# Kernel tuning notes

Hardware: AMD Instinct MI355X
Metric: run time of the kernel (lower is better)

Reference implementation:

```python
import jax, jax.numpy as jnp
import numpy as np

N_NODES = 20000
N_EDGES = 320000
N_GRAPHS = 32
C = 256
L = 4
IN_DIM = 739
EDGE_DIM = 2 * C + 6
LN_EPS = 1e-5


def _layernorm(x, g, b):
    mu = jnp.mean(x, axis=-1, keepdims=True)
    var = jnp.mean(jnp.square(x - mu), axis=-1, keepdims=True)
    return (x - mu) * jax.lax.rsqrt(var + LN_EPS) * g + b


def setup_inputs() -> dict:
    key = jax.random.key(0)
    ks = jax.random.split(key, 20)
    d = {}
    d["x"] = jax.random.normal(ks[0], (N_NODES, IN_DIM), jnp.float32)
    d["x_pos"] = jax.random.normal(ks[1], (N_NODES, 3), jnp.float32)
    d["edge_index"] = jax.random.randint(ks[2], (2, N_EDGES), 0, N_NODES, jnp.int32)
    d["batch"] = jnp.sort(jax.random.randint(ks[3], (N_NODES,), 0, N_GRAPHS, jnp.int32))
    s = 0.02
    d["dense_w"] = jax.random.normal(ks[4], (IN_DIM, C), jnp.float32) * s
    d["dense_b"] = jnp.zeros((C,), jnp.float32)
    d["d1_w"] = jax.random.normal(ks[5], (L, C, C), jnp.float32) * s
    d["d1_b"] = jnp.zeros((L, C), jnp.float32)
    d["ln1_g"] = jnp.ones((L, EDGE_DIM), jnp.float32)
    d["ln1_b"] = jnp.zeros((L, EDGE_DIM), jnp.float32)
    d["w1_w"] = jax.random.normal(ks[6], (L, EDGE_DIM, 4), jnp.float32) * s
    d["w1_b"] = jnp.zeros((L, 4), jnp.float32)
    d["ln2_g"] = jnp.ones((L, 4), jnp.float32)
    d["ln2_b"] = jnp.zeros((L, 4), jnp.float32)
    d["w2_w"] = jax.random.normal(ks[7], (L, 4, 1), jnp.float32) * s
    d["w2_b"] = jnp.zeros((L, 1), jnp.float32)
    d["d2_w"] = jax.random.normal(ks[8], (L, C, C), jnp.float32) * s
    d["d2_b"] = jnp.zeros((L, C), jnp.float32)
    d["head_w"] = jax.random.normal(ks[9], (C, 1), jnp.float32) * s
    d["head_b"] = jnp.zeros((1,), jnp.float32)
    return d


def reference(x, x_pos, edge_index, batch, dense_w, dense_b, d1_w, d1_b,
              ln1_g, ln1_b, w1_w, w1_b, ln2_g, ln2_b, w2_w, w2_b,
              d2_w, d2_b, head_w, head_b):
    n = x.shape[0]
    src, dst = edge_index[0], edge_index[1]
    h = x @ dense_w + dense_b  # [N, C]
    for l in range(d1_w.shape[0]):
        # message: dense1 -> GELU (dropout is identity in eval)
        m = jax.nn.gelu(h @ d1_w[l] + d1_b[l], approximate=False)  # [N, C]
        sx = m[src]                                                # [E, C]
        # edge-MLP input: [src_x, dst_x, src_pos, dst_pos]
        e = jnp.concatenate([sx, m[dst], x_pos[src], x_pos[dst]], axis=-1)  # [E, 2C+6]
        e = _layernorm(e, ln1_g[l], ln1_b[l])
        e = jax.nn.gelu(e @ w1_w[l] + w1_b[l], approximate=False)  # [E, 4]
        e = _layernorm(e, ln2_g[l], ln2_b[l])
        w = jax.nn.sigmoid(e @ w2_w[l] + w2_b[l])                  # [E, 1]
        agg = jax.ops.segment_sum(sx * w, dst, num_segments=n)     # [N, C]
        # update: dense2 -> GELU
        h = jax.nn.gelu(agg @ d2_w[l] + d2_b[l], approximate=False)
    # global mean pool over graphs
    sums = jax.ops.segment_sum(h, batch, num_segments=N_GRAPHS)           # [G, C]
    cnts = jax.ops.segment_sum(jnp.ones((n, 1), h.dtype), batch, num_segments=N_GRAPHS)
    pooled = sums / jnp.maximum(cnts, 1.0)
    return pooled @ head_w + head_b  # [G, 1]
```

## Files before the change

kernel.cpp:

```cpp
#include <hip/hip_runtime.h>
#include <math.h>

#define N_NODES 20000
#define N_EDGES 320000
#define N_GRAPHS 32
#define CDIM 256
#define IN_DIMV 739
#define KPAD_DENSE 768
#define ED_DIM 518
#define NLAYERS 4
#define LN_EPS 1e-5f
#define SCAN_BLOCKS ((N_NODES + 255) / 256)

typedef _Float16 f16x8 __attribute__((ext_vector_type(8)));
typedef _Float16 f16x4 __attribute__((ext_vector_type(4)));
typedef float f32x4 __attribute__((ext_vector_type(4)));

__device__ __forceinline__ float gelu_exact(float x) {
    return 0.5f * x * (1.f + erff(x * 0.7071067811865475f));
}

__device__ __forceinline__ void gll16(const void* g, void* l) {
    __builtin_amdgcn_global_load_lds((const __attribute__((address_space(1))) void*)g,
                                     (__attribute__((address_space(3))) void*)l, 16, 0, 0);
}

__global__ __launch_bounds__(256)
void prep_all(const float* __restrict__ ln1_g, const float* __restrict__ ln1_b,
              const float* __restrict__ w1_w, float* __restrict__ cw,
              float* __restrict__ SgSb,
              const float* __restrict__ dense_w, _Float16* __restrict__ wt_dense,
              const float* __restrict__ d1_w, const float* __restrict__ d2_w,
              _Float16* __restrict__ wt_sq, int* __restrict__ deg,
              float* __restrict__ sdot) {
    __shared__ float smem[2048 + 64];
    int b = blockIdx.x, tid = threadIdx.x;
    if (b < 79) {
        int i = b * 256 + tid;
        if (i < N_NODES) deg[i] = 0;
    } else if (b < 83) {
        int l = b - 79;
        float sg[4] = {0, 0, 0, 0}, sb[4] = {0, 0, 0, 0};
        for (int i = tid; i < ED_DIM; i += 256) {
            float g = ln1_g[l * ED_DIM + i];
            float bb = ln1_b[l * ED_DIM + i];
            float4 w = *(const float4*)&w1_w[(size_t)(l * ED_DIM + i) * 4];
            float4 c = make_float4(g * w.x, g * w.y, g * w.z, g * w.w);
            *(float4*)&cw[(size_t)(l * ED_DIM + i) * 4] = c;
            sg[0] += c.x; sg[1] += c.y; sg[2] += c.z; sg[3] += c.w;
            sb[0] += bb * w.x; sb[1] += bb * w.y; sb[2] += bb * w.z; sb[3] += bb * w.w;
        }
        for (int c = 0; c < 4; c++) { smem[tid * 8 + c] = sg[c]; smem[tid * 8 + 4 + c] = sb[c]; }
        __syncthreads();
        for (int s = 128; s > 0; s >>= 1) {
            if (tid < s)
                for (int c = 0; c < 8; c++) smem[tid * 8 + c] += smem[(tid + s) * 8 + c];
            __syncthreads();
        }
        if (tid < 8) SgSb[l * 8 + tid] = smem[tid];
    } else if (b < 275) {
        int q = b - 83;
        int kt = q >> 3, nt = q & 7;
        int i = tid >> 5, j = tid & 31;
        float* T = smem;
#pragma unroll
        for (int ii = 0; ii < 4; ii++) {
            int k = kt * 32 + i + ii * 8;
            T[(i + ii * 8) * 33 + j] = (k < IN_DIMV) ? dense_w[(size_t)k * 256 + nt * 32 + j] : 0.f;
        }
        __syncthreads();
#pragma unroll
        for (int ii = 0; ii < 4; ii++) {
            int n = nt * 32 + i + ii * 8;
            wt_dense[(size_t)n * KPAD_DENSE + kt * 32 + j] = (_Float16)T[j * 33 + i + ii * 8];
        }
    } else if (b < 787) {
        int q = b - 275;
        int z = q >> 6, kt = (q >> 3) & 7, nt = q & 7;
        const float* W = (z < 4) ? d1_w + (size_t)z * 65536 : d2_w + (size_t)(z - 4) * 65536;
        _Float16* O = wt_sq + (size_t)z * 65536;
        int i = tid >> 5, j = tid & 31;
        float* T = smem;
#pragma unroll
        for (int ii = 0; ii < 4; ii++)
            T[(i + ii * 8) * 33 + j] = W[(size_t)(kt * 32 + i + ii * 8) * 256 + nt * 32 + j];
        __syncthreads();
#pragma unroll
        for (int ii = 0; ii < 4; ii++)
            O[(size_t)(nt * 32 + i + ii * 8) * 256 + kt * 32 + j] = (_Float16)T[j * 33 + i + ii * 8];
    } else {
        int i = (b - 787) * 256 + tid;
        if (i < N_NODES) sdot[i] = 0.f;
    }
}

__global__ void hist_gstart_kernel(const int* __restrict__ ei, const int* __restrict__ batch,
                                   int* __restrict__ deg, int* __restrict__ gstart) {
    int e = blockIdx.x * 256 + threadIdx.x;
    if (e < N_EDGES) atomicAdd(&deg[ei[N_EDGES + e]], 1);
    if (e < N_NODES) {
        int b = batch[e];
        int bprev = (e == 0) ? -1 : batch[e - 1];
        for (int g = bprev + 1; g <= b; g++) gstart[g] = e;
        if (e == N_NODES - 1)
            for (int g = b + 1; g <= N_GRAPHS; g++) gstart[g] = N_NODES;
    }
}

__global__ __launch_bounds__(256)
void scan1_kernel(const int* __restrict__ deg, int* __restrict__ bsum) {
    __shared__ int red[256];
    int t = threadIdx.x;
    int i = blockIdx.x * 256 + t;
    red[t] = (i < N_NODES) ? deg[i] : 0;
    __syncthreads();
    for (int s = 128; s > 0; s >>= 1) {
        if (t < s) red[t] += red[t + s];
        __syncthreads();
    }
    if (t == 0) bsum[blockIdx.x] = red[0];
}

__global__ __launch_bounds__(128)
void scan2_kernel(const int* __restrict__ bsum, int* __restrict__ boff) {
    __shared__ int s[128];
    int t = threadIdx.x;
    int v = (t < SCAN_BLOCKS) ? bsum[t] : 0;
    s[t] = v;
    __syncthreads();
    for (int off = 1; off < 128; off <<= 1) {
        int o = (t >= off) ? s[t - off] : 0;
        __syncthreads();
        s[t] += o;
        __syncthreads();
    }
    if (t < SCAN_BLOCKS) boff[t] = s[t] - v;
}

__global__ __launch_bounds__(256)
void scan3_kernel(const int* __restrict__ deg, const int* __restrict__ boff,
                  int* __restrict__ row_start, int* __restrict__ cursor) {
    __shared__ int s[256];
    int t = threadIdx.x;
    int i = blockIdx.x * 256 + t;
    int v = (i < N_NODES) ? deg[i] : 0;
    s[t] = v;
    __syncthreads();
    for (int off = 1; off < 256; off <<= 1) {
        int o = (t >= off) ? s[t - off] : 0;
        __syncthreads();
        s[t] += o;
        __syncthreads();
    }
    int base = boff[blockIdx.x];
    int excl = base + s[t] - v;
    if (i < N_NODES) {
        row_start[i] = excl;
        cursor[i] = excl;
    }
    if (i == N_NODES - 1) row_start[N_NODES] = base + s[t];
}

__global__ void scatter_kernel(const int* __restrict__ ei, int* __restrict__ cursor,
                               int* __restrict__ csr_src, int* __restrict__ slot) {
    int e = blockIdx.x * 256 + threadIdx.x;
    if (e < N_EDGES) {
        int d = ei[N_EDGES + e];
        int pos = atomicAdd(&cursor[d], 1);
        csr_src[pos] = ei[e];
        slot[e] = pos;
    }
}

template <int KSTEPS, int AK, bool AFP32, bool GELU_ACT, bool DOT>
__global__ __launch_bounds__(256)
void gemm_v2(const void* __restrict__ Av, const _Float16* __restrict__ Bt,
             const float* __restrict__ bias, _Float16* __restrict__ C,
             const float* __restrict__ head_w, float* __restrict__ sdot) {
    constexpr int BSTR = KSTEPS * 64;
    __shared__ __align__(16) _Float16 Bs[3 * 128 * 64];
    __shared__ __align__(16) _Float16 As[(AFP32 ? 2 : 3) * 64 * 64];

    const int tid = threadIdx.x;
    const int row0 = blockIdx.x * 64;
    const int col0 = blockIdx.y * 128;
    const int wave = tid >> 6, lane = tid & 63;
    const int quad = lane >> 4, lrow = lane & 15;
    const int wrow = wave >> 1, wcol = wave & 1;

    const int sr = tid >> 3;
    const int scb = (tid & 7) << 4;
    const int srcCb = scb ^ ((sr & 7) << 4);

    const char* bsrc[4];
#pragma unroll
    for (int i = 0; i < 4; ++i)
        bsrc[i] = (const char*)Bt + (size_t)(col0 + i * 32 + sr) * (BSTR * 2) + srcCb;
    char* const bdst = (char*)&Bs[0] + tid * 16;

    const char* asrc[2];
    const float* afsrc[2];
    char* const adst = (char*)&As[0] + tid * 16;
    char* const adstw = (char*)&As[0] + sr * 128 + srcCb;
#pragma unroll
    for (int i = 0; i < 2; ++i) {
        int ar = row0 + i * 32 + sr;
        ar = (ar < N_NODES) ? ar : (N_NODES - 1);
        asrc[i] = (const char*)Av + (size_t)ar * (AK * 2) + srcCb;
        afsrc[i] = (const float*)Av + (size_t)ar * AK + (scb >> 1);
    }

    const int swz = ((lrow & 7) << 4) ^ (quad << 4);
    const int aro0 = (wrow * 32 + lrow) * 128;
    const int aro1 = aro0 + 2048;
    int bro[4];
#pragma unroll
    for (int t = 0; t < 4; ++t) bro[t] = (wcol * 64 + t * 16 + lrow) * 128;

    f32x4 acc[2][4];
#pragma unroll
    for (int i = 0; i < 2; ++i)
#pragma unroll
        for (int t = 0; t < 4; ++t) acc[i][t] = (f32x4){0.f, 0.f, 0.f, 0.f};

    float av[2][2][8];

    auto stage = [&](int j) {
        const int kb = j * 128;
        const int b3 = (j % 3) * 16384;
#pragma unroll
        for (int i = 0; i < 4; ++i) gll16(bsrc[i] + kb, bdst + b3 + i * 4096);
        if constexpr (!AFP32) {
            const int a3 = (j % 3) * 8192;
#pragma unroll
            for (int i = 0; i < 2; ++i) gll16(asrc[i] + kb, adst + a3 + i * 4096);
        } else {
            const int k0 = j * 64;
            const int p = j & 1;
            if ((j + 1) * 64 <= AK) {
#pragma unroll
                for (int jj = 0; jj < 8; ++jj) {
                    av[p][0][jj] = afsrc[0][k0 + jj];
                    av[p][1][jj] = afsrc[1][k0 + jj];
                }
            } else {
                const int kbase = k0 + (scb >> 1);
#pragma unroll
                for (int jj = 0; jj < 8; ++jj) {
                    av[p][0][jj] = (kbase + jj < AK) ? afsrc[0][k0 + jj] : 0.f;
                    av[p][1][jj] = (kbase + jj < AK) ? afsrc[1][k0 + jj] : 0.f;
                }
            }
        }
    };

    auto awrite = [&](int j) {
        if constexpr (AFP32) {
            const int ab = (j & 1) * 8192;
            const int p = j & 1;
            f16x8 v0, v1;
#pragma unroll
            for (int jj = 0; jj < 8; ++jj) {
                v0[jj] = (_Float16)av[p][0][jj];
                v1[jj] = (_Float16)av[p][1][jj];
            }
            *(f16x8*)(adstw + ab) = v0;
            *(f16x8*)(adstw + ab + 4096) = v1;
        }
    };

    auto compute = [&](int k) {
        const char* pa = (const char*)&As[0] + (AFP32 ? (k & 1) : (k % 3)) * 8192;
        const char* pb = (const char*)&Bs[0] + (k % 3) * 16384;
        __builtin_amdgcn_s_setprio(1);
#pragma unroll
        for (int h = 0; h < 2; ++h) {
            const int cbs = (h << 6) ^ swz;
            f16x8 af0 = *(const f16x8*)(pa + aro0 + cbs);
            f16x8 af1 = *(const f16x8*)(pa + aro1 + cbs);
#pragma unroll
            for (int t = 0; t < 4; ++t) {
                f16x8 bf = *(const f16x8*)(pb + bro[t] + cbs);
                acc[0][t] = __builtin_amdgcn_mfma_f32_16x16x32_f16(af0, bf, acc[0][t], 0, 0, 0);
                acc[1][t] = __builtin_amdgcn_mfma_f32_16x16x32_f16(af1, bf, acc[1][t], 0, 0, 0);
            }
        }
        __builtin_amdgcn_s_setprio(0);
    };

    stage(0);
    if constexpr (AFP32) {
        asm volatile("s_waitcnt vmcnt(0)" ::: "memory");
        __builtin_amdgcn_sched_barrier(0);
        awrite(0);
        stage(1);
        asm volatile("s_waitcnt lgkmcnt(0)" ::: "memory");
    } else {
        stage(1);
        asm volatile("s_waitcnt vmcnt(6) lgkmcnt(0)" ::: "memory");
    }
    __builtin_amdgcn_sched_barrier(0);
    __builtin_amdgcn_s_barrier();
    __builtin_amdgcn_sched_barrier(0);

#pragma unroll
    for (int k = 0; k < KSTEPS; ++k) {
        if (k + 2 < KSTEPS) stage(k + 2);
        compute(k);
        if (k + 1 < KSTEPS) {
            if (k + 2 < KSTEPS) {
                if constexpr (AFP32)
                    asm volatile("s_waitcnt vmcnt(8) lgkmcnt(0)" ::: "memory");
                else
                    asm volatile("s_waitcnt vmcnt(6) lgkmcnt(0)" ::: "memory");
            } else {
                asm volatile("s_waitcnt vmcnt(0) lgkmcnt(0)" ::: "memory");
            }
            __builtin_amdgcn_sched_barrier(0);
            if constexpr (AFP32) {
                awrite(k + 1);
                asm volatile("s_waitcnt lgkmcnt(0)" ::: "memory");
                __builtin_amdgcn_sched_barrier(0);
            }
            __builtin_amdgcn_s_barrier();
            __builtin_amdgcn_sched_barrier(0);
        }
    }

    const int orow = row0 + wrow * 32 + quad * 4;
    const int ocolb = col0 + wcol * 64 + lrow;
    if constexpr (DOT) {
        float dp0[4] = {0.f, 0.f, 0.f, 0.f}, dp1[4] = {0.f, 0.f, 0.f, 0.f};
#pragma unroll
        for (int t = 0; t < 4; ++t) {
            const int col = ocolb + t * 16;
            const float hw = head_w[col];
            const float bv = bias[col];
#pragma unroll
            for (int r = 0; r < 4; ++r) {
                dp0[r] += gelu_exact(acc[0][t][r] + bv) * hw;
                dp1[r] += gelu_exact(acc[1][t][r] + bv) * hw;
            }
        }
#pragma unroll
        for (int r = 0; r < 4; ++r) {
#pragma unroll
            for (int off = 1; off < 16; off <<= 1) {
                dp0[r] += __shfl_xor(dp0[r], off, 64);
                dp1[r] += __shfl_xor(dp1[r], off, 64);
            }
        }
        if (lrow == 0) {
#pragma unroll
            for (int r = 0; r < 4; ++r) {
                if (orow + r < N_NODES) atomicAdd(&sdot[orow + r], dp0[r]);
                if (orow + 16 + r < N_NODES) atomicAdd(&sdot[orow + 16 + r], dp1[r]);
            }
        }
    } else {
#pragma unroll
        for (int t = 0; t < 4; ++t) {
            const int col = ocolb + t * 16;
            const float bv = bias[col];
#pragma unroll
            for (int r = 0; r < 4; ++r) {
                float v0 = acc[0][t][r] + bv;
                float v1 = acc[1][t][r] + bv;
                if constexpr (GELU_ACT) { v0 = gelu_exact(v0); v1 = gelu_exact(v1); }
                if (orow + r < N_NODES)
                    C[(size_t)(orow + r) * 256 + col] = (_Float16)v0;
                if (orow + 16 + r < N_NODES)
                    C[(size_t)(orow + 16 + r) * 256 + col] = (_Float16)v1;
            }
        }
    }
}

__global__ __launch_bounds__(256)
void node_summary_kernel(const _Float16* __restrict__ m, const float* __restrict__ cw,
                         float* __restrict__ ns) {
    __shared__ __align__(16) float4 s_cw[512];
    int tid = threadIdx.x;
    for (int i = tid; i < 512; i += 256) s_cw[i] = *(const float4*)&cw[(size_t)i * 4];
    __syncthreads();
    int n = blockIdx.x * 4 + (tid >> 6);
    if (n >= N_NODES) return;
    int lane = tid & 63;
    f16x4 a4 = *(const f16x4*)&m[(size_t)n * CDIM + lane * 4];
    float av[4] = {(float)a4[0], (float)a4[1], (float)a4[2], (float)a4[3]};
    float Q1 = 0.f, Q2 = 0.f, P1[4] = {0, 0, 0, 0}, P2[4] = {0, 0, 0, 0};
#pragma unroll
    for (int j = 0; j < 4; j++) {
        Q1 += av[j];
        Q2 += av[j] * av[j];
        float4 c0 = s_cw[lane * 4 + j];
        float4 c1 = s_cw[256 + lane * 4 + j];
        P1[0] += av[j] * c0.x; P1[1] += av[j] * c0.y; P1[2] += av[j] * c0.z; P1[3] += av[j] * c0.w;
        P2[0] += av[j] * c1.x; P2[1] += av[j] * c1.y; P2[2] += av[j] * c1.z; P2[3] += av[j] * c1.w;
    }
#pragma unroll
    for (int off = 1; off < 64; off <<= 1) {
        Q1 += __shfl_xor(Q1, off, 64);
        Q2 += __shfl_xor(Q2, off, 64);
        P1[0] += __shfl_xor(P1[0], off, 64);
        P1[1] += __shfl_xor(P1[1], off, 64);
        P1[2] += __shfl_xor(P1[2], off, 64);
        P1[3] += __shfl_xor(P1[3], off, 64);
        P2[0] += __shfl_xor(P2[0], off, 64);
        P2[1] += __shfl_xor(P2[1], off, 64);
        P2[2] += __shfl_xor(P2[2], off, 64);
        P2[3] += __shfl_xor(P2[3], off, 64);
    }
    if (lane == 0) {
        float* p = &ns[(size_t)n * 12];
        *(float4*)p = make_float4(P1[0], P1[1], P1[2], P1[3]);
        *(float4*)(p + 4) = make_float4(P2[0], P2[1], P2[2], P2[3]);
        p[8] = Q1;
        p[9] = Q2;
    }
}

__global__ __launch_bounds__(256)
void edge_weight_kernel(const float* __restrict__ ns, const float* __restrict__ x_pos,
                        const int* __restrict__ ei, const float* __restrict__ cw,
                        const float* __restrict__ SgSb, const float* __restrict__ w1_b,
                        const float* __restrict__ ln2_g, const float* __restrict__ ln2_b,
                        const float* __restrict__ w2_w, const float* __restrict__ w2_b,
                        const int* __restrict__ slot, float* __restrict__ w_csr) {
    int e = blockIdx.x * 256 + threadIdx.x;
    if (e >= N_EDGES) return;
    int s = ei[e], d = ei[N_EDGES + e];
    const float* nss = &ns[(size_t)s * 12];
    const float* nsd = &ns[(size_t)d * 12];
    float4 p1 = *(const float4*)nss;
    float4 p2 = *(const float4*)(nsd + 4);
    float S1 = nss[8] + nsd[8];
    float S2 = nss[9] + nsd[9];
    float D[4] = {p1.x + p2.x, p1.y + p2.y, p1.z + p2.z, p1.w + p2.w};
    float ps[6];
    ps[0] = x_pos[(size_t)s * 3 + 0];
    ps[1] = x_pos[(size_t)s * 3 + 1];
    ps[2] = x_pos[(size_t)s * 3 + 2];
    ps[3] = x_pos[(size_t)d * 3 + 0];
    ps[4] = x_pos[(size_t)d * 3 + 1];
    ps[5] = x_pos[(size_t)d * 3 + 2];
#pragma unroll
    for (int k = 0; k < 6; k++) {
        S1 += ps[k];
        S2 += ps[k] * ps[k];
        float4 c = *(const float4*)&cw[(size_t)(512 + k) * 4];
        D[0] += ps[k] * c.x; D[1] += ps[k] * c.y; D[2] += ps[k] * c.z; D[3] += ps[k] * c.w;
    }
    const float inv = 1.f / 518.f;
    float mu = S1 * inv;
    float var = fmaf(-mu, mu, S2 * inv);
    float rstd = rsqrtf(var + LN_EPS);
    float t[4];
#pragma unroll
    for (int c = 0; c < 4; c++)
        t[c] = gelu_exact(rstd * (D[c] - mu * SgSb[c]) + SgSb[4 + c] + w1_b[c]);
    float mu2 = 0.25f * (t[0] + t[1] + t[2] + t[3]);
    float var2 = 0.25f * ((t[0] - mu2) * (t[0] - mu2) + (t[1] - mu2) * (t[1] - mu2) +
                          (t[2] - mu2) * (t[2] - mu2) + (t[3] - mu2) * (t[3] - mu2));
    float r2 = rsqrtf(var2 + LN_EPS);
    float z = w2_b[0];
#pragma unroll
    for (int c = 0; c < 4; c++)
        z += ((t[c] - mu2) * r2 * ln2_g[c] + ln2_b[c]) * w2_w[c];
    w_csr[slot[e]] = 1.f / (1.f + expf(-z));
}

__global__ __launch_bounds__(256)
void agg_kernel(const _Float16* __restrict__ m, const int* __restrict__ csr_src,
                const float* __restrict__ w_csr, const int* __restrict__ row_start,
                _Float16* __restrict__ agg) {
    int n = blockIdx.x * 4 + (threadIdx.x >> 6);
    if (n >= N_NODES) return;
    int lane = threadIdx.x & 63;
    int beg = row_start[n], end = row_start[n + 1];
    float a0 = 0.f, a1 = 0.f, a2 = 0.f, a3 = 0.f;
    int j = beg;
    for (; j + 8 <= end; j += 8) {
        int si[8];
        float wi[8];
#pragma unroll
        for (int u = 0; u < 8; u++) { si[u] = csr_src[j + u]; wi[u] = w_csr[j + u]; }
        f16x4 v[8];
#pragma unroll
        for (int u = 0; u < 8; u++) v[u] = *(const f16x4*)&m[(size_t)si[u] * CDIM + lane * 4];
#pragma unroll
        for (int u = 0; u < 8; u++) {
            a0 = fmaf(wi[u], (float)v[u][0], a0);
            a1 = fmaf(wi[u], (float)v[u][1], a1);
            a2 = fmaf(wi[u], (float)v[u][2], a2);
            a3 = fmaf(wi[u], (float)v[u][3], a3);
        }
    }
    for (; j < end; j++) {
        int s = csr_src[j];
        float w = w_csr[j];
        f16x4 v = *(const f16x4*)&m[(size_t)s * CDIM + lane * 4];
        a0 = fmaf(w, (float)v[0], a0);
        a1 = fmaf(w, (float)v[1], a1);
        a2 = fmaf(w, (float)v[2], a2);
        a3 = fmaf(w, (float)v[3], a3);
    }
    f16x4 o;
    o[0] = (_Float16)a0; o[1] = (_Float16)a1; o[2] = (_Float16)a2; o[3] = (_Float16)a3;
    *(f16x4*)&agg[(size_t)n * CDIM + lane * 4] = o;
}

__global__ __launch_bounds__(256)
void final_head_kernel(const float* __restrict__ sdot, const int* __restrict__ gstart,
                       const float* __restrict__ head_b, float* __restrict__ out) {
    int g = blockIdx.x;
    int t = threadIdx.x;
    int beg = gstart[g], end = gstart[g + 1];
    float s = 0.f;
    for (int i = beg + t; i < end; i += 256) s += sdot[i];
    __shared__ float red[256];
    red[t] = s;
    __syncthreads();
    for (int k = 128; k > 0; k >>= 1) {
        if (t < k) red[t] += red[t + k];
        __syncthreads();
    }
    if (t == 0) out[g] = red[0] / fmaxf((float)(end - beg), 1.f) + head_b[0];
}

extern "C" void kernel_launch(void* const* d_in, const int* in_sizes, int n_in,
                              void* d_out, int out_size, void* d_ws, size_t ws_size,
                              hipStream_t stream) {
    const float* x       = (const float*)d_in[0];
    const float* x_pos   = (const float*)d_in[1];
    const int*   ei      = (const int*)d_in[2];
    const int*   batch   = (const int*)d_in[3];
    const float* dense_w = (const float*)d_in[4];
    const float* dense_b = (const float*)d_in[5];
    const float* d1_w    = (const float*)d_in[6];
    const float* d1_b    = (const float*)d_in[7];
    const float* ln1_g   = (const float*)d_in[8];
    const float* ln1_b   = (const float*)d_in[9];
    const float* w1_w    = (const float*)d_in[10];
    const float* w1_b    = (const float*)d_in[11];
    const float* ln2_g   = (const float*)d_in[12];
    const float* ln2_b   = (const float*)d_in[13];
    const float* w2_w    = (const float*)d_in[14];
    const float* w2_b    = (const float*)d_in[15];
    const float* d2_w    = (const float*)d_in[16];
    const float* d2_b    = (const float*)d_in[17];
    const float* head_w  = (const float*)d_in[18];
    const float* head_b  = (const float*)d_in[19];
    float* out = (float*)d_out;

    _Float16* hbuf0 = (_Float16*)d_ws;
    _Float16* hbuf1 = hbuf0 + (size_t)N_NODES * CDIM;
    _Float16* wt_dense = hbuf1 + (size_t)N_NODES * CDIM;
    _Float16* wt_sq    = wt_dense + (size_t)256 * KPAD_DENSE;
    float* cw    = (float*)(wt_sq + (size_t)8 * 256 * 256);
    float* SgSb  = cw + (size_t)NLAYERS * ED_DIM * 4;
    float* ns    = SgSb + NLAYERS * 8;
    float* sdot  = ns + (size_t)N_NODES * 12;
    float* w_csr = sdot + N_NODES;
    int* gstart    = (int*)(w_csr + N_EDGES);
    int* deg       = gstart + N_GRAPHS + 1;
    int* row_start = deg + N_NODES;
    int* cursor    = row_start + N_NODES + 1;
    int* csr_src   = cursor + N_NODES;
    int* slot      = csr_src + N_EDGES;
    int* bsum      = slot + N_EDGES;
    int* boff      = bsum + SCAN_BLOCKS;

    prep_all<<<866, 256, 0, stream>>>(ln1_g, ln1_b, w1_w, cw, SgSb,
                                      dense_w, wt_dense, d1_w, d2_w, wt_sq, deg, sdot);

    hist_gstart_kernel<<<(N_EDGES + 255) / 256, 256, 0, stream>>>(ei, batch, deg, gstart);
    scan1_kernel<<<SCAN_BLOCKS, 256, 0, stream>>>(deg, bsum);
    scan2_kernel<<<1, 128, 0, stream>>>(bsum, boff);
    scan3_kernel<<<SCAN_BLOCKS, 256, 0, stream>>>(deg, boff, row_start, cursor);
    scatter_kernel<<<(N_EDGES + 255) / 256, 256, 0, stream>>>(ei, cursor, csr_src, slot);

    const dim3 G2((N_NODES + 63) / 64, 2);
    gemm_v2<12, IN_DIMV, true, false, false><<<G2, 256, 0, stream>>>(
        x, wt_dense, dense_b, hbuf0, nullptr, nullptr);

    _Float16* h = hbuf0;
    _Float16* other = hbuf1;
    for (int l = 0; l < NLAYERS; l++) {
        gemm_v2<4, CDIM, false, true, false><<<G2, 256, 0, stream>>>(
            h, wt_sq + (size_t)l * 65536, d1_b + l * CDIM, other, nullptr, nullptr);
        node_summary_kernel<<<(N_NODES + 3) / 4, 256, 0, stream>>>(
            other, cw + (size_t)l * ED_DIM * 4, ns);
        edge_weight_kernel<<<(N_EDGES + 255) / 256, 256, 0, stream>>>(
            ns, x_pos, ei, cw + (size_t)l * ED_DIM * 4, SgSb + l * 8, w1_b + l * 4,
            ln2_g + l * 4, ln2_b + l * 4, w2_w + l * 4, w2_b + l, slot, w_csr);
        agg_kernel<<<(N_NODES + 3) / 4, 256, 0, stream>>>(other, csr_src, w_csr, row_start, h);
        if (l < NLAYERS - 1) {
            gemm_v2<4, CDIM, false, true, false><<<G2, 256, 0, stream>>>(
                h, wt_sq + (size_t)(4 + l) * 65536, d2_b + l * CDIM, other, nullptr, nullptr);
        } else {
            gemm_v2<4, CDIM, false, true, true><<<G2, 256, 0, stream>>>(
                h, wt_sq + (size_t)(4 + l) * 65536, d2_b + l * CDIM, other, head_w, sdot);
        }
        _Float16* tmp = h; h = other; other = tmp;
    }

    final_head_kernel<<<N_GRAPHS, 256, 0, stream>>>(sdot, gstart, head_b, out);
}
```

Measured before the change: 554.5 us.

## Pre-convert x to padded fp16 and use direct-to-LDS loads in dense GEMM

Adds a separate kernel that converts the fp32 input features into a zero-padded fp16 buffer, so the first dense GEMM can stage A tiles with global_load_lds like the square GEMMs instead of doing register loads and in-kernel conversion. The GEMM template now takes a configurable pipeline depth, and the per-layer 256-wide GEMMs drop to double buffering. The conversion kernel adds an extra full read of x plus a write and re-read of the fp16 copy, and it uses per-element integer division.

```diff
diff --git a/kernel.cpp b/kernel.cpp
--- a/kernel.cpp
+++ b/kernel.cpp
@@ -23,6 +23,30 @@
 __device__ __forceinline__ void gll16(const void* g, void* l) {
     __builtin_amdgcn_global_load_lds((const __attribute__((address_space(1))) void*)g,
                                      (__attribute__((address_space(3))) void*)l, 16, 0, 0);
+}
+
+__global__ __launch_bounds__(256)
+void convert_x_kernel(const float* __restrict__ x, _Float16* __restrict__ xh) {
+    const int nquads = (N_NODES * IN_DIMV) / 4;
+    const int stride = gridDim.x * 256;
+    for (int q = blockIdx.x * 256 + threadIdx.x; q < nquads; q += stride) {
+        float4 v = ((const float4*)x)[q];
+        int base = q * 4;
+        float vv[4] = {v.x, v.y, v.z, v.w};
+#pragma unroll
+        for (int e = 0; e < 4; ++e) {
+            int idx = base + e;
+            int row = idx / IN_DIMV;
+            int col = idx - row * IN_DIMV;
+            xh[row * KPAD_DENSE + col] = (_Float16)vv[e];
+        }
+    }
+    const int npad = N_NODES * (KPAD_DENSE - IN_DIMV);
+    for (int p = blockIdx.x * 256 + threadIdx.x; p < npad; p += stride) {
+        int row = p / (KPAD_DENSE - IN_DIMV);
+        int col = IN_DIMV + (p - row * (KPAD_DENSE - IN_DIMV));
+        xh[row * KPAD_DENSE + col] = (_Float16)0.f;
+    }
 }
 
 __global__ __launch_bounds__(256)
@@ -172,14 +196,14 @@
     }
 }
 
-template <int KSTEPS, int AK, bool AFP32, bool GELU_ACT, bool DOT>
-__global__ __launch_bounds__(256)
-void gemm_v2(const void* __restrict__ Av, const _Float16* __restrict__ Bt,
+template <int KSTEPS, int NBUF, bool GELU_ACT, bool DOT>
+__global__ __launch_bounds__(256)
+void gemm_v3(const _Float16* __restrict__ A, const _Float16* __restrict__ Bt,
              const float* __restrict__ bias, _Float16* __restrict__ C,
              const float* __restrict__ head_w, float* __restrict__ sdot) {
-    constexpr int BSTR = KSTEPS * 64;
-    __shared__ __align__(16) _Float16 Bs[3 * 128 * 64];
-    __shared__ __align__(16) _Float16 As[(AFP32 ? 2 : 3) * 64 * 64];
+    constexpr int KDIM = KSTEPS * 64;
+    __shared__ __align__(16) _Float16 Bs[NBUF * 128 * 64];
+    __shared__ __align__(16) _Float16 As[NBUF * 64 * 64];
 
     const int tid = threadIdx.x;
     const int row0 = blockIdx.x * 64;
@@ -195,19 +219,16 @@
     const char* bsrc[4];
 #pragma unroll
     for (int i = 0; i < 4; ++i)
-        bsrc[i] = (const char*)Bt + (size_t)(col0 + i * 32 + sr) * (BSTR * 2) + srcCb;
+        bsrc[i] = (const char*)Bt + (size_t)(col0 + i * 32 + sr) * (KDIM * 2) + srcCb;
     char* const bdst = (char*)&Bs[0] + tid * 16;
 
     const char* asrc[2];
-    const float* afsrc[2];
     char* const adst = (char*)&As[0] + tid * 16;
-    char* const adstw = (char*)&As[0] + sr * 128 + srcCb;
 #pragma unroll
     for (int i = 0; i < 2; ++i) {
         int ar = row0 + i * 32 + sr;
         ar = (ar < N_NODES) ? ar : (N_NODES - 1);
-        asrc[i] = (const char*)Av + (size_t)ar * (AK * 2) + srcCb;
-        afsrc[i] = (const float*)Av + (size_t)ar * AK + (scb >> 1);
+        asrc[i] = (const char*)A + (size_t)ar * (KDIM * 2) + srcCb;
     }
 
     const int swz = ((lrow & 7) << 4) ^ (quad << 4);
@@ -223,55 +244,19 @@
 #pragma unroll
         for (int t = 0; t < 4; ++t) acc[i][t] = (f32x4){0.f, 0.f, 0.f, 0.f};
 
-    float av[2][2][8];
-
     auto stage = [&](int j) {
         const int kb = j * 128;
-        const int b3 = (j % 3) * 16384;
+        const int b3 = (j % NBUF) * 16384;
+        const int a3 = (j % NBUF) * 8192;
 #pragma unroll
         for (int i = 0; i < 4; ++i) gll16(bsrc[i] + kb, bdst + b3 + i * 4096);
-        if constexpr (!AFP32) {
-            const int a3 = (j % 3) * 8192;
-#pragma unroll
-            for (int i = 0; i < 2; ++i) gll16(asrc[i] + kb, adst + a3 + i * 4096);
-        } else {
-            const int k0 = j * 64;
-            const int p = j & 1;
-            if ((j + 1) * 64 <= AK) {
-#pragma unroll
-                for (int jj = 0; jj < 8; ++jj) {
-                    av[p][0][jj] = afsrc[0][k0 + jj];
-                    av[p][1][jj] = afsrc[1][k0 + jj];
-                }
-            } else {
-                const int kbase = k0 + (scb >> 1);
-#pragma unroll
-                for (int jj = 0; jj < 8; ++jj) {
-                    av[p][0][jj] = (kbase + jj < AK) ? afsrc[0][k0 + jj] : 0.f;
-                    av[p][1][jj] = (kbase + jj < AK) ? afsrc[1][k0 + jj] : 0.f;
-                }
-            }
-        }
+#pragma unroll
+        for (int i = 0; i < 2; ++i) gll16(asrc[i] + kb, adst + a3 + i * 4096);
     };
 
-    auto awrite = [&](int j) {
-        if constexpr (AFP32) {
-            const int ab = (j & 1) * 8192;
-            const int p = j & 1;
-            f16x8 v0, v1;
-#pragma unroll
-            for (int jj = 0; jj < 8; ++jj) {
-                v0[jj] = (_Float16)av[p][0][jj];
-                v1[jj] = (_Float16)av[p][1][jj];
-            }
-            *(f16x8*)(adstw + ab) = v0;
-            *(f16x8*)(adstw + ab + 4096) = v1;
-        }
-    };
-
     auto compute = [&](int k) {
-        const char* pa = (const char*)&As[0] + (AFP32 ? (k & 1) : (k % 3)) * 8192;
-        const char* pb = (const char*)&Bs[0] + (k % 3) * 16384;
+        const char* pa = (const char*)&As[0] + (k % NBUF) * 8192;
+        const char* pb = (const char*)&Bs[0] + (k % NBUF) * 16384;
         __builtin_amdgcn_s_setprio(1);
 #pragma unroll
         for (int h = 0; h < 2; ++h) {
@@ -289,15 +274,11 @@
     };
 
     stage(0);
-    if constexpr (AFP32) {
+    if (NBUF == 3 && KSTEPS > 1) {
+        stage(1);
+        asm volatile("s_waitcnt vmcnt(6)" ::: "memory");
+    } else {
         asm volatile("s_waitcnt vmcnt(0)" ::: "memory");
-        __builtin_amdgcn_sched_barrier(0);
-        awrite(0);
-        stage(1);
-        asm volatile("s_waitcnt lgkmcnt(0)" ::: "memory");
-    } else {
-        stage(1);
-        asm volatile("s_waitcnt vmcnt(6) lgkmcnt(0)" ::: "memory");
     }
     __builtin_amdgcn_sched_barrier(0);
     __builtin_amdgcn_s_barrier();
@@ -305,23 +286,15 @@
 
 #pragma unroll
     for (int k = 0; k < KSTEPS; ++k) {
-        if (k + 2 < KSTEPS) stage(k + 2);
+        const int nxt = k + NBUF - 1;
+        if (nxt < KSTEPS) stage(nxt);
         compute(k);
         if (k + 1 < KSTEPS) {
-            if (k + 2 < KSTEPS) {
-                if constexpr (AFP32)
-                    asm volatile("s_waitcnt vmcnt(8) lgkmcnt(0)" ::: "memory");
-                else
-                    asm volatile("s_waitcnt vmcnt(6) lgkmcnt(0)" ::: "memory");
-            } else {
+            if (NBUF == 3 && k + 2 < KSTEPS)
+                asm volatile("s_waitcnt vmcnt(6) lgkmcnt(0)" ::: "memory");
+            else
                 asm volatile("s_waitcnt vmcnt(0) lgkmcnt(0)" ::: "memory");
-            }
             __builtin_amdgcn_sched_barrier(0);
-            if constexpr (AFP32) {
-                awrite(k + 1);
-                asm volatile("s_waitcnt lgkmcnt(0)" ::: "memory");
-                __builtin_amdgcn_sched_barrier(0);
-            }
             __builtin_amdgcn_s_barrier();
             __builtin_amdgcn_sched_barrier(0);
         }
@@ -557,7 +530,8 @@
     _Float16* hbuf1 = hbuf0 + (size_t)N_NODES * CDIM;
     _Float16* wt_dense = hbuf1 + (size_t)N_NODES * CDIM;
     _Float16* wt_sq    = wt_dense + (size_t)256 * KPAD_DENSE;
-    float* cw    = (float*)(wt_sq + (size_t)8 * 256 * 256);
+    _Float16* x_h      = wt_sq + (size_t)8 * 256 * 256;
+    float* cw    = (float*)(x_h + (size_t)N_NODES * KPAD_DENSE);
     float* SgSb  = cw + (size_t)NLAYERS * ED_DIM * 4;
     float* ns    = SgSb + NLAYERS * 8;
     float* sdot  = ns + (size_t)N_NODES * 12;
@@ -573,6 +547,7 @@
 
     prep_all<<<866, 256, 0, stream>>>(ln1_g, ln1_b, w1_w, cw, SgSb,
                                       dense_w, wt_dense, d1_w, d2_w, wt_sq, deg, sdot);
+    convert_x_kernel<<<2048, 256, 0, stream>>>(x, x_h);
 
     hist_gstart_kernel<<<(N_EDGES + 255) / 256, 256, 0, stream>>>(ei, batch, deg, gstart);
     scan1_kernel<<<SCAN_BLOCKS, 256, 0, stream>>>(deg, bsum);
@@ -581,13 +556,13 @@
     scatter_kernel<<<(N_EDGES + 255) / 256, 256, 0, stream>>>(ei, cursor, csr_src, slot);
 
     const dim3 G2((N_NODES + 63) / 64, 2);
-    gemm_v2<12, IN_DIMV, true, false, false><<<G2, 256, 0, stream>>>(
-        x, wt_dense, dense_b, hbuf0, nullptr, nullptr);
+    gemm_v3<12, 3, false, false><<<G2, 256, 0, stream>>>(
+        x_h, wt_dense, dense_b, hbuf0, nullptr, nullptr);
 
     _Float16* h = hbuf0;
     _Float16* other = hbuf1;
     for (int l = 0; l < NLAYERS; l++) {
-        gemm_v2<4, CDIM, false, true, false><<<G2, 256, 0, stream>>>(
+        gemm_v3<4, 2, true, false><<<G2, 256, 0, stream>>>(
             h, wt_sq + (size_t)l * 65536, d1_b + l * CDIM, other, nullptr, nullptr);
         node_summary_kernel<<<(N_NODES + 3) / 4, 256, 0, stream>>>(
             other, cw + (size_t)l * ED_DIM * 4, ns);
@@ -596,10 +571,10 @@
             ln2_g + l * 4, ln2_b + l * 4, w2_w + l * 4, w2_b + l, slot, w_csr);
         agg_kernel<<<(N_NODES + 3) / 4, 256, 0, stream>>>(other, csr_src, w_csr, row_start, h);
         if (l < NLAYERS - 1) {
-            gemm_v2<4, CDIM, false, true, false><<<G2, 256, 0, stream>>>(
+            gemm_v3<4, 2, true, false><<<G2, 256, 0, stream>>>(
                 h, wt_sq + (size_t)(4 + l) * 65536, d2_b + l * CDIM, other, nullptr, nullptr);
         } else {
-            gemm_v2<4, CDIM, false, true, true><<<G2, 256, 0, stream>>>(
+            gemm_v3<4, 2, true, true><<<G2, 256, 0, stream>>>(
                 h, wt_sq + (size_t)(4 + l) * 65536, d2_b + l * CDIM, other, head_w, sdot);
         }
         _Float16* tmp = h; h = other; other = tmp;
```

Result: faster. 524.6 us (-5.4%).
